# Performance work log

Measured on AMD Instinct MI355X. Metric: run time of the kernel, lower is better.

## Reference

```python
import jax, jax.numpy as jnp
import numpy as np

N = 50000   # total nodes (50 graphs x 1000 nodes)
E = 500000  # total edges (avg degree 10)
G = 50      # number of graphs in the batch
IN = 128    # in_dim
H = 4       # attn_head
HID = [64, 128]  # graph_hiddens
SLOPE = 0.2      # negative_slope


def setup_inputs() -> dict:
    key = jax.random.key(0)
    ks = jax.random.split(key, 12)
    nodes_per_g = N // G
    edges_per_g = E // G
    # edges stay inside their own graph block (batched-graph structure)
    off = (jnp.arange(E) // edges_per_g) * nodes_per_g
    edge_src = (jax.random.randint(ks[0], (E,), 0, nodes_per_g) + off).astype(jnp.int32)
    edge_dst = (jax.random.randint(ks[1], (E,), 0, nodes_per_g) + off).astype(jnp.int32)
    node_graph = (jnp.arange(N) // nodes_per_g).astype(jnp.int32)

    def lin(k, i, o):
        return (jax.random.normal(k, (i, o), jnp.float32) / np.sqrt(i)).astype(jnp.float32)

    return dict(
        x=jax.random.normal(ks[2], (N, IN), jnp.float32),
        edge_src=edge_src, edge_dst=edge_dst, node_graph=node_graph,
        Wl1=lin(ks[3], IN, H * HID[0]), bl1=jnp.zeros((H * HID[0],), jnp.float32),
        Wr1=lin(ks[4], IN, H * HID[0]), br1=jnp.zeros((H * HID[0],), jnp.float32),
        attn1=jax.random.normal(ks[5], (H, HID[0]), jnp.float32) * 0.1,
        Wl2=lin(ks[6], HID[0], H * HID[1]), bl2=jnp.zeros((H * HID[1],), jnp.float32),
        Wr2=lin(ks[7], HID[0], H * HID[1]), br2=jnp.zeros((H * HID[1],), jnp.float32),
        attn2=jax.random.normal(ks[8], (H, HID[1]), jnp.float32) * 0.1,
        gate_w=lin(ks[9], HID[1], 1), gate_b=jnp.zeros((1,), jnp.float32),
    )


def _gat_layer(x, src, dst, Wl, bl, Wr, br, attn, n_heads, d_out):
    """DGL GATv2Conv (share_weights=False, no dropout) + maxpool over heads."""
    n = x.shape[0]
    fs = (x @ Wl + bl).reshape(n, n_heads, d_out)  # fc_src -> [N,H,D]
    fd = (x @ Wr + br).reshape(n, n_heads, d_out)  # fc_dst -> [N,H,D]
    # per-edge GATv2 logits: attn . leaky_relu(fs_u + fd_v)
    e = jax.nn.leaky_relu(fs[src] + fd[dst], SLOPE)      # [E,H,D]
    logits = jnp.einsum('ehd,hd->eh', e, attn)           # [E,H]
    # edge softmax over incoming edges of each destination node
    m = jax.ops.segment_max(logits, dst, num_segments=n)  # [N,H]
    a = jnp.exp(logits - m[dst])
    s = jax.ops.segment_sum(a, dst, num_segments=n)
    alpha = a / s[dst]                                   # [E,H]
    out = jax.ops.segment_sum(alpha[:, :, None] * fs[src], dst, num_segments=n)  # [N,H,D]
    # MaxPool1d(attn_head) over the head dimension -> [N,D]
    return out.max(axis=1)


def reference(x, edge_src, edge_dst, node_graph,
              Wl1, bl1, Wr1, br1, attn1,
              Wl2, bl2, Wr2, br2, attn2,
              gate_w, gate_b):
    h = _gat_layer(x, edge_src, edge_dst, Wl1, bl1, Wr1, br1, attn1, H, HID[0])
    h = _gat_layer(h, edge_src, edge_dst, Wl2, bl2, Wr2, br2, attn2, H, HID[1])
    # GlobalAttentionPooling: softmax(gate_nn(h)) per graph, weighted sum
    gate = (h @ gate_w + gate_b)[:, 0]                      # [N]
    gm = jax.ops.segment_max(gate, node_graph, num_segments=G)
    ga = jnp.exp(gate - gm[node_graph])
    gs = jax.ops.segment_sum(ga, node_graph, num_segments=G)
    alpha = (ga / gs[node_graph])[:, None]                  # [N,1]
    return jax.ops.segment_sum(alpha * h, node_graph, num_segments=G)  # [G, HID[1]]
```

## Files before the change

kernel.cpp:

```cpp
#include <hip/hip_runtime.h>
#include <hip/hip_bf16.h>


#define NN 50000
#define EE 500000
#define GG 50
#define NPG 1000
#define HH 4

typedef unsigned short ushort_t;
typedef unsigned int uint_t;
typedef __attribute__((ext_vector_type(8))) short bf16x8;
typedef __attribute__((ext_vector_type(4))) float f32x4;

__device__ __forceinline__ ushort_t bf16r(float f) {
  __hip_bfloat16 h = __float2bfloat16(f);
  return *reinterpret_cast<ushort_t*>(&h);
}

__device__ __forceinline__ float2 up2(uint_t u) {
  return make_float2(__uint_as_float(u << 16), __uint_as_float(u & 0xffff0000u));
}


__global__ void count_dst(const int* __restrict__ dst, int* __restrict__ counts) {
  int i = blockIdx.x * 256 + threadIdx.x;
  if (i < EE) atomicAdd(&counts[dst[i]], 1);
}

__global__ void scan_block(const int* __restrict__ in, int* __restrict__ out,
                           int* __restrict__ bsum, int n) {
  __shared__ int tmp[256];
  int t = threadIdx.x;
  int i = blockIdx.x * 256 + t;
  int v = (i < n) ? in[i] : 0;
  tmp[t] = v;
  __syncthreads();
  for (int off = 1; off < 256; off <<= 1) {
    int a = (t >= off) ? tmp[t - off] : 0;
    __syncthreads();
    tmp[t] += a;
    __syncthreads();
  }
  if (i < n) out[i] = tmp[t] - v;
  if (t == 255) bsum[blockIdx.x] = tmp[t];
}

__global__ void scan_bsum(int* __restrict__ bsum, int nb) {
  __shared__ int tmp[256];
  int t = threadIdx.x;
  int v = (t < nb) ? bsum[t] : 0;
  tmp[t] = v;
  __syncthreads();
  for (int off = 1; off < 256; off <<= 1) {
    int a = (t >= off) ? tmp[t - off] : 0;
    __syncthreads();
    tmp[t] += a;
    __syncthreads();
  }
  if (t < nb) bsum[t] = tmp[t] - v;
}

__global__ void scan_add(int* __restrict__ out, const int* __restrict__ bsum,
                         int* __restrict__ cursor, int n) {
  int i = blockIdx.x * 256 + threadIdx.x;
  if (i < n) {
    out[i] += bsum[blockIdx.x];
    cursor[i] = 0;
  }
}

__global__ void scatter_edges(const int* __restrict__ src, const int* __restrict__ dst,
                              const int* __restrict__ rowstart, int* __restrict__ cursor,
                              int* __restrict__ csr_src) {
  int i = blockIdx.x * 256 + threadIdx.x;
  if (i < EE) {
    int d = dst[i];
    int p = atomicAdd(&cursor[d], 1);
    csr_src[rowstart[d] + p] = src[i];
  }
}


__global__ void prep_w_all(const float* __restrict__ Wl1, const float* __restrict__ Wr1,
                           const float* __restrict__ Wl2, const float* __restrict__ Wr2,
                           ushort_t* __restrict__ BW1, ushort_t* __restrict__ BW2) {
  int i = blockIdx.x * 256 + threadIdx.x;
  if (i < 512 * 128) {
    int n = i >> 7, k = i & 127;
    const float* W = (n < 256) ? Wl1 : Wr1;
    BW1[i] = bf16r(W[(size_t)k * 256 + (n & 255)]);
  } else {
    int j = i - 512 * 128;
    int n = j >> 6, k = j & 63;
    const float* W = (n < 512) ? Wl2 : Wr2;
    BW2[j] = bf16r(W[(size_t)k * 512 + (n & 511)]);
  }
}


template<int KDIM, bool AF32>
__global__ __launch_bounds__(256)
void gemm_mfma(const float* __restrict__ Af, const ushort_t* __restrict__ Ab,
               const ushort_t* __restrict__ BW,
               const float* __restrict__ bl, const float* __restrict__ br, int nhalf,
               ushort_t* __restrict__ C, int nstride) {
  constexpr int RS = 72;
  __shared__ __align__(16) ushort_t As[128 * RS];
  __shared__ __align__(16) ushort_t Bs[128 * RS];
  const int t = threadIdx.x;
  const int m0 = blockIdx.x * 128, n0 = blockIdx.y * 128;
  const int lane = t & 63, wv = t >> 6;
  const int l16 = lane & 15, quad = lane >> 4;

  f32x4 acc[2][8];
#pragma unroll
  for (int b = 0; b < 2; ++b)
#pragma unroll
    for (int n = 0; n < 8; ++n) acc[b][n] = (f32x4){0.f, 0.f, 0.f, 0.f};

  for (int k0 = 0; k0 < KDIM; k0 += 64) {
    __syncthreads();
    if (AF32) {
      const int r = t >> 4, c4 = t & 15;
#pragma unroll
      for (int p = 0; p < 8; ++p) {
        int m = m0 + r + p * 16;
        int ms = (m < NN) ? m : NN - 1;
        float4 v = *(const float4*)(Af + (size_t)ms * KDIM + k0 + c4 * 4);
        uint2 pk;
        pk.x = (uint_t)bf16r(v.x) | ((uint_t)bf16r(v.y) << 16);
        pk.y = (uint_t)bf16r(v.z) | ((uint_t)bf16r(v.w) << 16);
        *(uint2*)(As + (r + p * 16) * RS + c4 * 4) = pk;
      }
    } else {
      const int r = t >> 3, seg = t & 7;
#pragma unroll
      for (int p = 0; p < 4; ++p) {
        int m = m0 + r + p * 32;
        int ms = (m < NN) ? m : NN - 1;
        *(uint4*)(As + (r + p * 32) * RS + seg * 8) =
            *(const uint4*)(Ab + (size_t)ms * KDIM + k0 + seg * 8);
      }
    }
    {
      const int r = t >> 3, seg = t & 7;
#pragma unroll
      for (int p = 0; p < 4; ++p) {
        *(uint4*)(Bs + (r + p * 32) * RS + seg * 8) =
            *(const uint4*)(BW + (size_t)(n0 + r + p * 32) * KDIM + k0 + seg * 8);
      }
    }
    __syncthreads();
#pragma unroll
    for (int kk = 0; kk < 2; ++kk) {
      bf16x8 a[2];
#pragma unroll
      for (int b = 0; b < 2; ++b)
        a[b] = *(const bf16x8*)(As + (wv * 32 + b * 16 + l16) * RS + kk * 32 + quad * 8);
#pragma unroll
      for (int n = 0; n < 8; ++n) {
        bf16x8 bb = *(const bf16x8*)(Bs + (n * 16 + l16) * RS + kk * 32 + quad * 8);
        acc[0][n] = __builtin_amdgcn_mfma_f32_16x16x32_bf16(a[0], bb, acc[0][n], 0, 0, 0);
        acc[1][n] = __builtin_amdgcn_mfma_f32_16x16x32_bf16(a[1], bb, acc[1][n], 0, 0, 0);
      }
    }
  }
  const float* bp = (n0 < nhalf) ? bl : br;
  const int nb = (n0 < nhalf) ? n0 : n0 - nhalf;
#pragma unroll
  for (int n = 0; n < 8; ++n) {
    const int col = n0 + n * 16 + l16;
    const float bv = bp[nb + n * 16 + l16];
#pragma unroll
    for (int b = 0; b < 2; ++b) {
      const int rowb = m0 + wv * 32 + b * 16 + quad * 4;
#pragma unroll
      for (int r = 0; r < 4; ++r) {
        if (rowb + r < NN)
          C[(size_t)(rowb + r) * nstride + col] = bf16r(acc[b][n][r] + bv);
      }
    }
  }
}


template<int N32> struct UV;
template<> struct UV<2> { typedef uint2 T; };
template<> struct UV<4> { typedef uint4 T; };

#define SLOTS_X 1563
#define BLK_X   391
#define GAT_GRID (BLK_X * 8)

template<int D, int STRIDE, bool OUTBF, bool GATE>
__global__ __launch_bounds__(256)
void gat_layer(const ushort_t* __restrict__ fsb, const ushort_t* __restrict__ fdb,
               const float* __restrict__ attn,
               const int* __restrict__ rowstart, const int* __restrict__ deg,
               const int* __restrict__ csr_src,
               float4* __restrict__ out4, ushort_t* __restrict__ outb,
               const float* __restrict__ gw, float* __restrict__ gate) {
  constexpr int DPL = D / 16;
  constexpr int NU  = DPL / 2;
  constexpr int NV4 = DPL / 4;
  constexpr int D4  = D / 4;
  typedef typename UV<NU>::T LT;

  const int b    = blockIdx.x;
  const int xcd  = b & 7;
  const int bi   = b >> 3;
  const int lane = threadIdx.x & 63;
  const int wvid = threadIdx.x >> 6;
  const int h    = lane >> 4;
  const int g16  = lane & 15;
  const int foff = h * D + g16 * DPL;

  float at[DPL];
#pragma unroll
  for (int i = 0; i < DPL; ++i) at[i] = attn[foff + i];
  float gwv[DPL];
  if constexpr (GATE) {
#pragma unroll
    for (int i = 0; i < DPL; ++i) gwv[i] = gw[g16 * DPL + i];
  }

  for (int j = 0; j < 4; ++j) {
    const int ls = bi + j * BLK_X;
    if (ls >= SLOTS_X) break;
    const int slot = xcd * SLOTS_X + ls;
    if (slot >= NN / 4) break;
    const int v = (slot << 2) + wvid;

    float fdv[DPL];
    {
      LT raw = *reinterpret_cast<const LT*>(fdb + (size_t)v * STRIDE + foff);
      const uint_t* rw = reinterpret_cast<const uint_t*>(&raw);
#pragma unroll
      for (int q = 0; q < NU; ++q) {
        float2 f = up2(rw[q]);
        fdv[2 * q] = f.x; fdv[2 * q + 1] = f.y;
      }
    }
    const int start = rowstart[v];
    const int n     = deg[v];
    const int* cp   = csr_src + start;

    float s = 0.f;
    float acc[DPL];
#pragma unroll
    for (int i = 0; i < DPL; ++i) acc[i] = 0.f;

    for (int c0 = 0; c0 < n; c0 += 64) {
      int idx = 0;
      if (c0 + lane < n) idx = cp[c0 + lane];
      const int rem = n - c0;
      const int en = (rem < 64) ? rem : 64;
      for (int e = 0; e < en; ++e) {
        const int u = __shfl(idx, e);
        LT raw = *reinterpret_cast<const LT*>(fsb + (size_t)u * STRIDE + foff);
        const uint_t* rw = reinterpret_cast<const uint_t*>(&raw);
        float f0[DPL];
#pragma unroll
        for (int q = 0; q < NU; ++q) {
          float2 f = up2(rw[q]);
          f0[2 * q] = f.x; f0[2 * q + 1] = f.y;
        }
        float p = 0.f;
#pragma unroll
        for (int i = 0; i < DPL; ++i) {
          float tt = f0[i] + fdv[i];
          p = fmaf(fmaxf(tt, 0.2f * tt), at[i], p);
        }
        p += __shfl_xor(p, 1);
        p += __shfl_xor(p, 2);
        p += __shfl_xor(p, 4);
        p += __shfl_xor(p, 8);
        const float w = __expf(p);
        s += w;
#pragma unroll
        for (int i = 0; i < DPL; ++i) acc[i] = fmaf(w, f0[i], acc[i]);
      }
    }

    const float rs = (n > 0) ? (1.0f / s) : 0.f;
#pragma unroll
    for (int i = 0; i < DPL; ++i) {
      acc[i] *= rs;
      acc[i] = fmaxf(acc[i], __shfl_xor(acc[i], 16));
      acc[i] = fmaxf(acc[i], __shfl_xor(acc[i], 32));
    }
    if constexpr (GATE) {
      float gp = 0.f;
#pragma unroll
      for (int i = 0; i < DPL; ++i) gp = fmaf(acc[i], gwv[i], gp);
      gp += __shfl_xor(gp, 1);  gp += __shfl_xor(gp, 2);  gp += __shfl_xor(gp, 4);
      gp += __shfl_xor(gp, 8);  gp += __shfl_xor(gp, 16); gp += __shfl_xor(gp, 32);
      if (lane == 0) gate[v] = gp * 0.25f;
    }
    if (h == 0) {
      if constexpr (OUTBF) {
        ushort4 o;
        o.x = bf16r(acc[0]); o.y = bf16r(acc[1]); o.z = bf16r(acc[2]); o.w = bf16r(acc[3]);
        *reinterpret_cast<ushort4*>(outb + (size_t)v * D + g16 * 4) = o;
      } else {
#pragma unroll
        for (int i = 0; i < NV4; ++i)
          out4[(size_t)v * D4 + g16 * NV4 + i] =
              make_float4(acc[4 * i], acc[4 * i + 1], acc[4 * i + 2], acc[4 * i + 3]);
      }
    }
  }
}


__global__ __launch_bounds__(256)
void pool_soft(const float* __restrict__ gate, float* __restrict__ alpha) {
  const int g = blockIdx.x, t = threadIdx.x;
  const int lane = t & 63, w = t >> 6;
  __shared__ float red[4];
  __shared__ float finm, fins;
  const float* gp = gate + g * NPG;

  float m = -__builtin_inff();
  for (int i = t; i < NPG; i += 256) m = fmaxf(m, gp[i]);
  m = fmaxf(m, __shfl_xor(m, 1));  m = fmaxf(m, __shfl_xor(m, 2));
  m = fmaxf(m, __shfl_xor(m, 4));  m = fmaxf(m, __shfl_xor(m, 8));
  m = fmaxf(m, __shfl_xor(m, 16)); m = fmaxf(m, __shfl_xor(m, 32));
  if (lane == 0) red[w] = m;
  __syncthreads();
  if (t == 0) finm = fmaxf(fmaxf(red[0], red[1]), fmaxf(red[2], red[3]));
  __syncthreads();
  const float gm = finm;

  float s = 0.f;
  for (int i = t; i < NPG; i += 256) s += __expf(gp[i] - gm);
  s += __shfl_xor(s, 1);  s += __shfl_xor(s, 2);  s += __shfl_xor(s, 4);
  s += __shfl_xor(s, 8);  s += __shfl_xor(s, 16); s += __shfl_xor(s, 32);
  if (lane == 0) red[w] = s;
  __syncthreads();
  if (t == 0) fins = 1.0f / (red[0] + red[1] + red[2] + red[3]);
  __syncthreads();
  const float inv = fins;

  for (int i = t; i < NPG; i += 256)
    alpha[g * NPG + i] = __expf(gp[i] - gm) * inv;
}

#define PCH 8
__global__ __launch_bounds__(128)
void pool_acc(const float* __restrict__ h2, const float* __restrict__ alpha,
              float* __restrict__ out) {
  const int g = blockIdx.x / PCH;
  const int c = blockIdx.x % PCH;
  const int d = threadIdx.x;
  const int n0 = g * NPG + c * (NPG / PCH);
  float acc = 0.f;
#pragma unroll 4
  for (int i = 0; i < NPG / PCH; ++i)
    acc = fmaf(alpha[n0 + i], h2[(size_t)(n0 + i) * 128 + d], acc);
  atomicAdd(&out[g * 128 + d], acc);
}


extern "C" void kernel_launch(void* const* d_in, const int* in_sizes, int n_in,
                              void* d_out, int out_size, void* d_ws, size_t ws_size,
                              hipStream_t stream) {
  const float* x        = (const float*)d_in[0];
  const int*   edge_src = (const int*)d_in[1];
  const int*   edge_dst = (const int*)d_in[2];
  const float* Wl1   = (const float*)d_in[4];
  const float* bl1   = (const float*)d_in[5];
  const float* Wr1   = (const float*)d_in[6];
  const float* br1   = (const float*)d_in[7];
  const float* attn1 = (const float*)d_in[8];
  const float* Wl2   = (const float*)d_in[9];
  const float* bl2   = (const float*)d_in[10];
  const float* Wr2   = (const float*)d_in[11];
  const float* br2   = (const float*)d_in[12];
  const float* attn2 = (const float*)d_in[13];
  const float* gate_w = (const float*)d_in[14];
  float* out = (float*)d_out;

  ushort_t* fsd1 = (ushort_t*)d_ws;
  ushort_t* fsd2 = fsd1;
  ushort_t* h1b  = fsd2 + (size_t)NN * 1024;
  float* h2      = (float*)(h1b + (size_t)NN * 64);
  float* gate    = h2 + (size_t)NN * 128;
  float* alpha   = gate + NN;
  ushort_t* BW1  = (ushort_t*)(alpha + NN);
  ushort_t* BW2  = BW1 + 512 * 128;
  int* counts   = (int*)(BW2 + 1024 * 64);
  int* rowstart = counts + NN;
  int* cursor   = rowstart + NN;
  int* csr_src  = cursor + NN;
  int* bsum     = csr_src + EE;

  hipMemsetAsync(counts, 0, NN * sizeof(int), stream);
  hipMemsetAsync(d_out, 0, (size_t)GG * 128 * sizeof(float), stream);

  const int nbN = (NN + 255) / 256;
  const int nbE = (EE + 255) / 256;
  const int MB  = (NN + 127) / 128;

  prep_w_all<<<(512 * 128 + 1024 * 64) / 256, 256, 0, stream>>>(
      Wl1, Wr1, Wl2, Wr2, BW1, BW2);

  count_dst<<<nbE, 256, 0, stream>>>(edge_dst, counts);
  scan_block<<<nbN, 256, 0, stream>>>(counts, rowstart, bsum, NN);
  scan_bsum<<<1, 256, 0, stream>>>(bsum, nbN);
  scan_add<<<nbN, 256, 0, stream>>>(rowstart, bsum, cursor, NN);
  scatter_edges<<<nbE, 256, 0, stream>>>(edge_src, edge_dst, rowstart, cursor, csr_src);

  gemm_mfma<128, true><<<dim3(MB, 4), 256, 0, stream>>>(
      x, nullptr, BW1, bl1, br1, 256, fsd1, 512);
  gat_layer<64, 512, true, false><<<GAT_GRID, 256, 0, stream>>>(
      fsd1, fsd1 + 256, attn1, rowstart, counts, csr_src,
      nullptr, h1b, nullptr, nullptr);
  gemm_mfma<64, false><<<dim3(MB, 8), 256, 0, stream>>>(
      nullptr, h1b, BW2, bl2, br2, 512, fsd2, 1024);
  gat_layer<128, 1024, false, true><<<GAT_GRID, 256, 0, stream>>>(
      fsd2, fsd2 + 512, attn2, rowstart, counts, csr_src,
      (float4*)h2, nullptr, gate_w, gate);

  pool_soft<<<GG, 256, 0, stream>>>(gate, alpha);
  pool_acc<<<GG * PCH, 128, 0, stream>>>(h2, alpha, out);
}
```

Measured before the change: 406.5 us.

## Map one block per 4-node slot and vectorize GAT edge math with packed f32x2

The GAT aggregation kernel now launches one block per group of four destination nodes instead of looping each block over up to four slots. This adds blocks but shortens each one, keeping the XCD-aware slot striping. Per-edge math is rewritten with two-wide float vectors so the compiler can emit packed FMA and max instructions. Neighbor indices are now read directly from the CSR array per edge instead of being batch-loaded and shuffled across the wavefront, which trades shuffles for scalar-broadcast loads.

Result: no change. 408.7 us (+0.5%).

```diff
diff --git a/kernel.cpp b/kernel.cpp
--- a/kernel.cpp
+++ b/kernel.cpp
@@ -12,14 +12,18 @@
 typedef unsigned int uint_t;
 typedef __attribute__((ext_vector_type(8))) short bf16x8;
 typedef __attribute__((ext_vector_type(4))) float f32x4;
+typedef __attribute__((ext_vector_type(2))) float f32x2;
 
 __device__ __forceinline__ ushort_t bf16r(float f) {
   __hip_bfloat16 h = __float2bfloat16(f);
   return *reinterpret_cast<ushort_t*>(&h);
 }
 
-__device__ __forceinline__ float2 up2(uint_t u) {
-  return make_float2(__uint_as_float(u << 16), __uint_as_float(u & 0xffff0000u));
+__device__ __forceinline__ f32x2 up2v(uint_t u) {
+  f32x2 r;
+  r.x = __uint_as_float(u << 16);
+  r.y = __uint_as_float(u & 0xffff0000u);
+  return r;
 }
 
 
@@ -189,9 +193,8 @@
 template<> struct UV<2> { typedef uint2 T; };
 template<> struct UV<4> { typedef uint4 T; };
 
-#define SLOTS_X 1563
-#define BLK_X   391
-#define GAT_GRID (BLK_X * 8)
+#define GAT_SLOTS ((NN / 4 + 7) / 8)
+#define GAT_GRID  (GAT_SLOTS * 8)
 
 template<int D, int STRIDE, bool OUTBF, bool GATE>
 __global__ __launch_bounds__(256)
@@ -208,107 +211,100 @@
   typedef typename UV<NU>::T LT;
 
   const int b    = blockIdx.x;
-  const int xcd  = b & 7;
-  const int bi   = b >> 3;
+  const int slot = (b & 7) * GAT_SLOTS + (b >> 3);
+  if (slot >= NN / 4) return;
   const int lane = threadIdx.x & 63;
   const int wvid = threadIdx.x >> 6;
+  const int v    = (slot << 2) + wvid;
   const int h    = lane >> 4;
   const int g16  = lane & 15;
   const int foff = h * D + g16 * DPL;
 
-  float at[DPL];
-#pragma unroll
-  for (int i = 0; i < DPL; ++i) at[i] = attn[foff + i];
-  float gwv[DPL];
+  f32x2 at2[NU], fd2[NU], gw2[NU];
+  {
+    const float* ap = attn + foff;
+#pragma unroll
+    for (int j = 0; j < NU; ++j) { at2[j].x = ap[2 * j]; at2[j].y = ap[2 * j + 1]; }
+    LT raw = *reinterpret_cast<const LT*>(fdb + (size_t)v * STRIDE + foff);
+    const uint_t* rw = reinterpret_cast<const uint_t*>(&raw);
+#pragma unroll
+    for (int j = 0; j < NU; ++j) fd2[j] = up2v(rw[j]);
+    if constexpr (GATE) {
+      const float* gp = gw + g16 * DPL;
+#pragma unroll
+      for (int j = 0; j < NU; ++j) { gw2[j].x = gp[2 * j]; gw2[j].y = gp[2 * j + 1]; }
+    }
+  }
+  const int start = rowstart[v];
+  const int n     = deg[v];
+  const int* cp   = csr_src + start;
+
+  float s = 0.f;
+  f32x2 acc2[NU];
+#pragma unroll
+  for (int j = 0; j < NU; ++j) acc2[j] = (f32x2){0.f, 0.f};
+
+  for (int e = 0; e < n; ++e) {
+    const int u = cp[e];
+    LT raw = *reinterpret_cast<const LT*>(fsb + (size_t)u * STRIDE + foff);
+    const uint_t* rw = reinterpret_cast<const uint_t*>(&raw);
+    f32x2 f0[NU];
+#pragma unroll
+    for (int j = 0; j < NU; ++j) f0[j] = up2v(rw[j]);
+    f32x2 p2 = (f32x2){0.f, 0.f};
+#pragma unroll
+    for (int j = 0; j < NU; ++j) {
+      f32x2 t = f0[j] + fd2[j];
+      f32x2 l = __builtin_elementwise_max(t, t * 0.2f);
+      p2 = __builtin_elementwise_fma(l, at2[j], p2);
+    }
+    float p = p2.x + p2.y;
+    p += __shfl_xor(p, 1);
+    p += __shfl_xor(p, 2);
+    p += __shfl_xor(p, 4);
+    p += __shfl_xor(p, 8);
+    const float w = __expf(p);
+    s += w;
+    const f32x2 wv2 = {w, w};
+#pragma unroll
+    for (int j = 0; j < NU; ++j)
+      acc2[j] = __builtin_elementwise_fma(wv2, f0[j], acc2[j]);
+  }
+
+  const float rs = (n > 0) ? (1.0f / s) : 0.f;
+  float acc[DPL];
+#pragma unroll
+  for (int j = 0; j < NU; ++j) {
+    acc[2 * j]     = acc2[j].x * rs;
+    acc[2 * j + 1] = acc2[j].y * rs;
+  }
+#pragma unroll
+  for (int i = 0; i < DPL; ++i) {
+    acc[i] = fmaxf(acc[i], __shfl_xor(acc[i], 16));
+    acc[i] = fmaxf(acc[i], __shfl_xor(acc[i], 32));
+  }
   if constexpr (GATE) {
-#pragma unroll
-    for (int i = 0; i < DPL; ++i) gwv[i] = gw[g16 * DPL + i];
-  }
-
-  for (int j = 0; j < 4; ++j) {
-    const int ls = bi + j * BLK_X;
-    if (ls >= SLOTS_X) break;
-    const int slot = xcd * SLOTS_X + ls;
-    if (slot >= NN / 4) break;
-    const int v = (slot << 2) + wvid;
-
-    float fdv[DPL];
-    {
-      LT raw = *reinterpret_cast<const LT*>(fdb + (size_t)v * STRIDE + foff);
-      const uint_t* rw = reinterpret_cast<const uint_t*>(&raw);
-#pragma unroll
-      for (int q = 0; q < NU; ++q) {
-        float2 f = up2(rw[q]);
-        fdv[2 * q] = f.x; fdv[2 * q + 1] = f.y;
-      }
-    }
-    const int start = rowstart[v];
-    const int n     = deg[v];
-    const int* cp   = csr_src + start;
-
-    float s = 0.f;
-    float acc[DPL];
-#pragma unroll
-    for (int i = 0; i < DPL; ++i) acc[i] = 0.f;
-
-    for (int c0 = 0; c0 < n; c0 += 64) {
-      int idx = 0;
-      if (c0 + lane < n) idx = cp[c0 + lane];
-      const int rem = n - c0;
-      const int en = (rem < 64) ? rem : 64;
-      for (int e = 0; e < en; ++e) {
-        const int u = __shfl(idx, e);
-        LT raw = *reinterpret_cast<const LT*>(fsb + (size_t)u * STRIDE + foff);
-        const uint_t* rw = reinterpret_cast<const uint_t*>(&raw);
-        float f0[DPL];
-#pragma unroll
-        for (int q = 0; q < NU; ++q) {
-          float2 f = up2(rw[q]);
-          f0[2 * q] = f.x; f0[2 * q + 1] = f.y;
-        }
-        float p = 0.f;
-#pragma unroll
-        for (int i = 0; i < DPL; ++i) {
-          float tt = f0[i] + fdv[i];
-          p = fmaf(fmaxf(tt, 0.2f * tt), at[i], p);
-        }
-        p += __shfl_xor(p, 1);
-        p += __shfl_xor(p, 2);
-        p += __shfl_xor(p, 4);
-        p += __shfl_xor(p, 8);
-        const float w = __expf(p);
-        s += w;
-#pragma unroll
-        for (int i = 0; i < DPL; ++i) acc[i] = fmaf(w, f0[i], acc[i]);
-      }
-    }
-
-    const float rs = (n > 0) ? (1.0f / s) : 0.f;
-#pragma unroll
-    for (int i = 0; i < DPL; ++i) {
-      acc[i] *= rs;
-      acc[i] = fmaxf(acc[i], __shfl_xor(acc[i], 16));
-      acc[i] = fmaxf(acc[i], __shfl_xor(acc[i], 32));
-    }
-    if constexpr (GATE) {
-      float gp = 0.f;
-#pragma unroll
-      for (int i = 0; i < DPL; ++i) gp = fmaf(acc[i], gwv[i], gp);
-      gp += __shfl_xor(gp, 1);  gp += __shfl_xor(gp, 2);  gp += __shfl_xor(gp, 4);
-      gp += __shfl_xor(gp, 8);  gp += __shfl_xor(gp, 16); gp += __shfl_xor(gp, 32);
-      if (lane == 0) gate[v] = gp * 0.25f;
-    }
-    if (h == 0) {
-      if constexpr (OUTBF) {
-        ushort4 o;
-        o.x = bf16r(acc[0]); o.y = bf16r(acc[1]); o.z = bf16r(acc[2]); o.w = bf16r(acc[3]);
-        *reinterpret_cast<ushort4*>(outb + (size_t)v * D + g16 * 4) = o;
-      } else {
-#pragma unroll
-        for (int i = 0; i < NV4; ++i)
-          out4[(size_t)v * D4 + g16 * NV4 + i] =
-              make_float4(acc[4 * i], acc[4 * i + 1], acc[4 * i + 2], acc[4 * i + 3]);
-      }
+    f32x2 g2 = (f32x2){0.f, 0.f};
+#pragma unroll
+    for (int j = 0; j < NU; ++j) {
+      f32x2 a2; a2.x = acc[2 * j]; a2.y = acc[2 * j + 1];
+      g2 = __builtin_elementwise_fma(a2, gw2[j], g2);
+    }
+    float gp = g2.x + g2.y;
+    gp += __shfl_xor(gp, 1);  gp += __shfl_xor(gp, 2);  gp += __shfl_xor(gp, 4);
+    gp += __shfl_xor(gp, 8);  gp += __shfl_xor(gp, 16); gp += __shfl_xor(gp, 32);
+    if (lane == 0) gate[v] = gp * 0.25f;
+  }
+  if (h == 0) {
+    if constexpr (OUTBF) {
+      ushort4 o;
+      o.x = bf16r(acc[0]); o.y = bf16r(acc[1]); o.z = bf16r(acc[2]); o.w = bf16r(acc[3]);
+      *reinterpret_cast<ushort4*>(outb + (size_t)v * D + g16 * 4) = o;
+    } else {
+#pragma unroll
+      for (int i = 0; i < NV4; ++i)
+        out4[(size_t)v * D4 + g16 * NV4 + i] =
+            make_float4(acc[4 * i], acc[4 * i + 1], acc[4 * i + 2], acc[4 * i + 3]);
     }
   }
 }
```
